# Optimization experiments

Measured on AMD Instinct MI355X. Metric: run time of the kernel, lower is better.

The kernel has to match this reference:

```python
import jax, jax.numpy as jnp
import numpy as np

HIDDEN = 512
B, H, W = 8, 48, 48
SCALE = 1.0 / np.sqrt(HIDDEN).astype(np.float32)


def conv1x1(x, w, b):
    # x: [B, C, H, W], w: [O, C], b: [O]  (1x1 Conv2d == channel matmul)
    return jnp.einsum('bchw,oc->bohw', x, w) + b[None, :, None, None]


def setup_inputs() -> dict:
    key = jax.random.key(0)
    ks = jax.random.split(key, 10)
    s = 1.0 / np.sqrt(HIDDEN)
    return {
        'locx': jax.random.normal(ks[0], (B, HIDDEN, H, W), dtype=jnp.float32),
        'glox': jax.random.normal(ks[1], (B, HIDDEN, H, W), dtype=jnp.float32),
        'Wq': jax.random.normal(ks[2], (HIDDEN, HIDDEN), dtype=jnp.float32) * s,
        'bq': jax.random.normal(ks[3], (HIDDEN,), dtype=jnp.float32) * 0.01,
        'Wk': jax.random.normal(ks[4], (HIDDEN, HIDDEN), dtype=jnp.float32) * s,
        'bk': jax.random.normal(ks[5], (HIDDEN,), dtype=jnp.float32) * 0.01,
        'Wv': jax.random.normal(ks[6], (HIDDEN, HIDDEN), dtype=jnp.float32) * s,
        'bv': jax.random.normal(ks[7], (HIDDEN,), dtype=jnp.float32) * 0.01,
        'Wo': jax.random.normal(ks[8], (HIDDEN, HIDDEN), dtype=jnp.float32) * s,
        'bo': jax.random.normal(ks[9], (HIDDEN,), dtype=jnp.float32) * 0.01,
    }


def reference(locx, glox, Wq, bq, Wk, bk, Wv, bv, Wo, bo):
    b, c, h, w = locx.shape
    # 1x1 conv projections
    q = conv1x1(locx, Wq, bq).reshape(b, c, h * w)   # [B, C, N]
    k = conv1x1(glox, Wk, bk).reshape(b, c, -1)      # [B, C, M]
    v = conv1x1(glox, Wv, bv).reshape(b, c, -1)      # [B, C, M]
    # scores = Q^T K / sqrt(hidden)  -> [B, N, M]
    scores = jnp.einsum('bcn,bcm->bnm', q, k) * SCALE
    probs = jax.nn.softmax(scores, axis=-1)           # dropout rate 0.0 -> identity
    # context = probs @ V^T -> [B, N, C] -> [B, C, H, H]
    ctx = jnp.einsum('bnm,bcm->bcn', probs, v).reshape(b, c, h, h)
    out = conv1x1(ctx, Wo, bo)                        # proj dropout 0.0 -> identity
    return out
```

## Files before the change

### kernel.cpp

```cpp
#include <hip/hip_runtime.h>
#include <hip/hip_bf16.h>

typedef __attribute__((ext_vector_type(4))) float f32x4;
typedef __attribute__((ext_vector_type(8))) short bf16x8;
typedef __attribute__((ext_vector_type(4))) short s16x4;

#define C_DIM 512
#define N_PIX 2304
#define N_BATCH 8
#define ATT_SCALE 0.04419417382415922f
#define NJB 18

typedef __attribute__((address_space(3))) unsigned int lds_u32;
typedef const __attribute__((address_space(1))) unsigned int glob_u32;

__device__ __forceinline__ void gl2lds16(const __hip_bfloat16* g, __hip_bfloat16* l)
{
    __builtin_amdgcn_global_load_lds((glob_u32*)g, (lds_u32*)l, 16, 0, 0);
}

template<int NS>
__global__ __launch_bounds__(256)
void s_vp(const __hip_bfloat16* __restrict__ Qt, const __hip_bfloat16* __restrict__ Kt,
          __hip_bfloat16* __restrict__ Pu, float* __restrict__ rp,
          const __hip_bfloat16* __restrict__ wo, const __hip_bfloat16* __restrict__ Vt,
          __hip_bfloat16* __restrict__ Vp, int bz_off, long sPu)
{
    __shared__ __hip_bfloat16 As[128 * 64];
    __shared__ __hip_bfloat16 Bs[128 * 64];

    const int lin = blockIdx.x;
    const int bz  = lin % NS + bz_off;
    const int t   = lin / NS;
    const bool is_s = (t < 324);

    int ib, jb;
    const __hip_bfloat16 *A, *B;
    __hip_bfloat16* D;
    float scale;
    const long sQ = (long)N_PIX * C_DIM;
    if (is_s) {
        ib = t / 18; jb = t % 18;
        A = Qt + (size_t)bz * sQ;
        B = Kt + (size_t)bz * sQ;
        D = Pu + (size_t)bz * (size_t)sPu;
        scale = ATT_SCALE;
    } else {
        int u = t - 324;
        ib = u / 18; jb = u % 18;
        A = wo;
        B = Vt + (size_t)bz * sQ;
        D = Vp + (size_t)bz * sQ;
        scale = 1.f;
    }
    const int i0 = ib * 128;
    const int j0 = jb * 128;

    const int tid  = threadIdx.x;
    const int lane = tid & 63;
    const int wave = tid >> 6;

    const int lrow = lane >> 3;
    const int lcs  = (lane & 7) ^ lrow;
    const __hip_bfloat16* ga = A + (size_t)(i0 + wave * 32 + lrow) * C_DIM + lcs * 8;
    const __hip_bfloat16* gb = B + (size_t)(j0 + wave * 32 + lrow) * C_DIM + lcs * 8;
    __hip_bfloat16* la = As + wave * 32 * 64;
    __hip_bfloat16* lb = Bs + wave * 32 * 64;

    const int fr = lane & 15;
    const int fq = lane >> 4;
    const int sw = fr & 7;
    const int wi = (wave >> 1) * 64;
    const int wj = (wave & 1) * 64;

    f32x4 acc[4][4];
#pragma unroll
    for (int a = 0; a < 4; ++a)
#pragma unroll
        for (int b = 0; b < 4; ++b)
            acc[a][b] = (f32x4){0.f, 0.f, 0.f, 0.f};

    for (int k0 = 0; k0 < C_DIM; k0 += 64) {
#pragma unroll
        for (int ss = 0; ss < 4; ++ss) {
            gl2lds16(ga + (size_t)ss * 8 * C_DIM + k0, la + ss * 8 * 64);
            gl2lds16(gb + (size_t)ss * 8 * C_DIM + k0, lb + ss * 8 * 64);
        }
        __syncthreads();

#pragma unroll
        for (int kk = 0; kk < 2; ++kk) {
            bf16x8 af[4], bfr[4];
            const int ca = ((kk * 4 + fq) ^ sw) << 3;
#pragma unroll
            for (int tt = 0; tt < 4; ++tt) {
                af[tt]  = *(const bf16x8*)(&As[(wi + tt * 16 + fr) * 64 + ca]);
                bfr[tt] = *(const bf16x8*)(&Bs[(wj + tt * 16 + fr) * 64 + ca]);
            }
#pragma unroll
            for (int a = 0; a < 4; ++a)
#pragma unroll
                for (int b = 0; b < 4; ++b)
                    acc[a][b] = __builtin_amdgcn_mfma_f32_16x16x32_bf16(
                        af[a], bfr[b], acc[a][b], 0, 0, 0);
        }
        __syncthreads();
    }

    const int orow = fq * 4;

    if (is_s) {
        float rpart[4][4];
#pragma unroll
        for (int a = 0; a < 4; ++a)
#pragma unroll
            for (int r = 0; r < 4; ++r)
                rpart[a][r] = 0.f;
#pragma unroll
        for (int a = 0; a < 4; ++a) {
            int ibx = i0 + wi + a * 16 + orow;
#pragma unroll
            for (int b = 0; b < 4; ++b) {
                int j = j0 + wj + b * 16 + fr;
#pragma unroll
                for (int r = 0; r < 4; ++r) {
                    float v = __expf(acc[a][b][r] * scale);
                    rpart[a][r] += v;
                    D[(size_t)(ibx + r) * N_PIX + j] = __float2bfloat16(v);
                }
            }
        }
#pragma unroll
        for (int m = 1; m < 16; m <<= 1)
#pragma unroll
            for (int a = 0; a < 4; ++a)
#pragma unroll
                for (int r = 0; r < 4; ++r)
                    rpart[a][r] += __shfl_xor(rpart[a][r], m);
        float* rsl = (float*)As;
        if (fr == 0) {
#pragma unroll
            for (int a = 0; a < 4; ++a)
#pragma unroll
                for (int r = 0; r < 4; ++r)
                    rsl[wave * 64 + a * 16 + orow + r] = rpart[a][r];
        }
        __syncthreads();
        if (tid < 128) {
            int half = tid >> 6, rr = tid & 63;
            float sm = rsl[(half * 2) * 64 + rr] + rsl[(half * 2 + 1) * 64 + rr];
            rp[((size_t)jb * N_BATCH + bz) * N_PIX + i0 + tid] = sm;
        }
    } else {
#pragma unroll
        for (int a = 0; a < 4; ++a) {
            int ibx = i0 + wi + a * 16 + orow;
#pragma unroll
            for (int b = 0; b < 4; ++b) {
                int j = j0 + wj + b * 16 + fr;
#pragma unroll
                for (int r = 0; r < 4; ++r)
                    D[(size_t)(ibx + r) * N_PIX + j] = __float2bfloat16(acc[a][b][r]);
            }
        }
    }
}

template<int NS>
__global__ __launch_bounds__(256)
void pv_out(const __hip_bfloat16* __restrict__ Vp, const __hip_bfloat16* __restrict__ Pu,
            float* __restrict__ out, const float* __restrict__ bo,
            const float* __restrict__ rp, int bz_off, long sPu)
{
    __shared__ __hip_bfloat16 As[64 * 64];
    __shared__ __hip_bfloat16 Bs[128 * 64];

    const int lin = blockIdx.x;
    const int bz  = lin % NS + bz_off;
    const int t   = lin / NS;
    const int ib  = t % 8;
    const int jb  = t / 8;
    const int i0  = ib * 64;
    const int j0  = jb * 128;

    const long sCN = (long)C_DIM * N_PIX;
    const __hip_bfloat16* A = Vp + (size_t)bz * sCN;
    const __hip_bfloat16* B = Pu + (size_t)bz * (size_t)sPu;
    float* D = out + (size_t)bz * sCN;

    const int tid  = threadIdx.x;
    const int lane = tid & 63;
    const int wave = tid >> 6;

    const int lrow = lane >> 3;
    const int lcs  = (lane & 7) ^ lrow;
    const __hip_bfloat16* ga = A + (size_t)(i0 + wave * 16 + lrow) * N_PIX + lcs * 8;
    const __hip_bfloat16* gb = B + (size_t)(j0 + wave * 32 + lrow) * N_PIX + lcs * 8;
    __hip_bfloat16* la = As + wave * 16 * 64;
    __hip_bfloat16* lb = Bs + wave * 32 * 64;

    const int fr = lane & 15;
    const int fq = lane >> 4;
    const int sw = fr & 7;
    const int wi = (wave >> 1) * 32;
    const int wj = (wave & 1) * 64;

    f32x4 acc[2][4];
#pragma unroll
    for (int a = 0; a < 2; ++a)
#pragma unroll
        for (int b = 0; b < 4; ++b)
            acc[a][b] = (f32x4){0.f, 0.f, 0.f, 0.f};

    for (int k0 = 0; k0 < N_PIX; k0 += 64) {
#pragma unroll
        for (int ss = 0; ss < 2; ++ss)
            gl2lds16(ga + (size_t)ss * 8 * N_PIX + k0, la + ss * 8 * 64);
#pragma unroll
        for (int ss = 0; ss < 4; ++ss)
            gl2lds16(gb + (size_t)ss * 8 * N_PIX + k0, lb + ss * 8 * 64);
        __syncthreads();

#pragma unroll
        for (int kk = 0; kk < 2; ++kk) {
            bf16x8 af[2], bfr[4];
            const int ca = ((kk * 4 + fq) ^ sw) << 3;
#pragma unroll
            for (int tt = 0; tt < 2; ++tt)
                af[tt]  = *(const bf16x8*)(&As[(wi + tt * 16 + fr) * 64 + ca]);
#pragma unroll
            for (int tt = 0; tt < 4; ++tt)
                bfr[tt] = *(const bf16x8*)(&Bs[(wj + tt * 16 + fr) * 64 + ca]);
#pragma unroll
            for (int a = 0; a < 2; ++a)
#pragma unroll
                for (int b = 0; b < 4; ++b)
                    acc[a][b] = __builtin_amdgcn_mfma_f32_16x16x32_bf16(
                        af[a], bfr[b], acc[a][b], 0, 0, 0);
        }
        __syncthreads();
    }

    const int orow = fq * 4;
    float rjv[4];
#pragma unroll
    for (int b = 0; b < 4; ++b) {
        int j = j0 + wj + b * 16 + fr;
        float s = 0.f;
#pragma unroll
        for (int jj = 0; jj < NJB; ++jj)
            s += rp[((size_t)jj * N_BATCH + bz) * N_PIX + j];
        rjv[b] = 1.f / s;
    }

#pragma unroll
    for (int a = 0; a < 2; ++a) {
        int ibx = i0 + wi + a * 16 + orow;
#pragma unroll
        for (int r = 0; r < 4; ++r) {
            float bi = bo[ibx + r];
#pragma unroll
            for (int b = 0; b < 4; ++b) {
                int j = j0 + wj + b * 16 + fr;
                D[(size_t)(ibx + r) * N_PIX + j] = acc[a][b][r] * rjv[b] + bi;
            }
        }
    }
}

__global__ __launch_bounds__(256)
void proj_qkv(const __hip_bfloat16* __restrict__ Xl,
              const __hip_bfloat16* __restrict__ Xg,
              const __hip_bfloat16* __restrict__ wgt,
              const float* __restrict__ bq, const float* __restrict__ bk,
              const float* __restrict__ bv,
              __hip_bfloat16* __restrict__ QKV)
{
    __shared__ __hip_bfloat16 As[128 * 64];
    __shared__ __hip_bfloat16 Bs[128 * 64];

    const int lin = blockIdx.x;
    const int s   = lin % 24;
    const int bz  = s & 7;
    const int mat = s >> 3;
    const int t   = lin / 24;
    const int j0  = (t & 3) * 128;
    const int i0  = (t >> 2) * 128;

    const __hip_bfloat16* Ab = ((mat == 0) ? Xl : Xg) + (size_t)bz * N_PIX * C_DIM;
    const __hip_bfloat16* Bb = wgt + (size_t)mat * C_DIM * C_DIM;
    const float* bias = (mat == 0) ? bq : (mat == 1) ? bk : bv;
    __hip_bfloat16* D = QKV + ((size_t)mat * N_BATCH + bz) * N_PIX * C_DIM;

    const int tid  = threadIdx.x;
    const int lane = tid & 63;
    const int wave = tid >> 6;

    const int lrow = lane >> 3;
    const int lcs  = (lane & 7) ^ lrow;
    const __hip_bfloat16* ga = Ab + (size_t)(i0 + wave * 32 + lrow) * C_DIM + lcs * 8;
    const __hip_bfloat16* gb = Bb + (size_t)(j0 + wave * 32 + lrow) * C_DIM + lcs * 8;
    __hip_bfloat16* la = As + wave * 32 * 64;
    __hip_bfloat16* lb = Bs + wave * 32 * 64;

    const int fr = lane & 15;
    const int fq = lane >> 4;
    const int sw = fr & 7;
    const int wi = (wave >> 1) * 64;
    const int wj = (wave & 1) * 64;

    f32x4 acc[4][4];
#pragma unroll
    for (int a = 0; a < 4; ++a)
#pragma unroll
        for (int b = 0; b < 4; ++b)
            acc[a][b] = (f32x4){0.f, 0.f, 0.f, 0.f};

    for (int k0 = 0; k0 < C_DIM; k0 += 64) {
#pragma unroll
        for (int ss = 0; ss < 4; ++ss) {
            gl2lds16(ga + (size_t)ss * 8 * C_DIM + k0, la + ss * 8 * 64);
            gl2lds16(gb + (size_t)ss * 8 * C_DIM + k0, lb + ss * 8 * 64);
        }
        __syncthreads();

#pragma unroll
        for (int kk = 0; kk < 2; ++kk) {
            bf16x8 af[4], bfr[4];
            const int ca = ((kk * 4 + fq) ^ sw) << 3;
#pragma unroll
            for (int tt = 0; tt < 4; ++tt) {
                af[tt]  = *(const bf16x8*)(&As[(wi + tt * 16 + fr) * 64 + ca]);
                bfr[tt] = *(const bf16x8*)(&Bs[(wj + tt * 16 + fr) * 64 + ca]);
            }
#pragma unroll
            for (int a = 0; a < 4; ++a)
#pragma unroll
                for (int b = 0; b < 4; ++b)
                    acc[a][b] = __builtin_amdgcn_mfma_f32_16x16x32_bf16(
                        af[a], bfr[b], acc[a][b], 0, 0, 0);
        }
        __syncthreads();
    }

    const int orow = fq * 4;
#pragma unroll
    for (int a = 0; a < 4; ++a) {
        int ibx = i0 + wi + a * 16 + orow;
#pragma unroll
        for (int b = 0; b < 4; ++b) {
            int j = j0 + wj + b * 16 + fr;
            float bj = bias[j];
#pragma unroll
            for (int r = 0; r < 4; ++r)
                D[(size_t)(ibx + r) * C_DIM + j] = __float2bfloat16(acc[a][b][r] + bj);
        }
    }
}

__global__ __launch_bounds__(256)
void prep(const float* __restrict__ locx, const float* __restrict__ glox,
          __hip_bfloat16* __restrict__ Xl, __hip_bfloat16* __restrict__ Xg,
          const float* __restrict__ w0, const float* __restrict__ w1,
          const float* __restrict__ w2, const float* __restrict__ w3,
          __hip_bfloat16* __restrict__ wgt)
{
    const int lin = blockIdx.x;
    const int tid = threadIdx.x;

    if (lin < 4608) {
        __shared__ float t[64 * 65];
        const int z  = lin & 15;
        const int t2 = lin >> 4;
        const int c0 = (t2 & 7) * 64;
        const int n0 = (t2 >> 3) * 64;
        const size_t b = z & 7;
        const float* Xb = ((z < 8) ? locx : glox) + b * (size_t)C_DIM * N_PIX;
        __hip_bfloat16* Xt = (z < 8) ? Xl : Xg;

        const int n_l = tid & 63;
        const int c_b = tid >> 6;
#pragma unroll
        for (int s = 0; s < 16; ++s) {
            int c_l = c_b + s * 4;
            t[c_l * 65 + n_l] = Xb[(size_t)(c0 + c_l) * N_PIX + n0 + n_l];
        }
        __syncthreads();

        const int cc = (tid & 7) * 8;
        const int nb = tid >> 3;
#pragma unroll
        for (int it = 0; it < 2; ++it) {
            int n2 = nb + it * 32;
            union { __hip_bfloat16 h[8]; int4 v; } u;
#pragma unroll
            for (int w = 0; w < 8; ++w)
                u.h[w] = __float2bfloat16(t[(cc + w) * 65 + n2]);
            *(int4*)(&Xt[(b * N_PIX + n0 + n2) * C_DIM + c0 + cc]) = u.v;
        }
    } else {
        const int idx = lin - 4608;
        const int w   = idx >> 8;
        const float* srcs[4] = {w0, w1, w2, w3};
        const int i = ((idx & 255) * 256 + tid) * 4;
        float4 f = *(const float4*)(srcs[w] + i);
        union { __hip_bfloat16 h[4]; s16x4 q; } u;
        u.h[0] = __float2bfloat16(f.x);
        u.h[1] = __float2bfloat16(f.y);
        u.h[2] = __float2bfloat16(f.z);
        u.h[3] = __float2bfloat16(f.w);
        *(s16x4*)(wgt + (size_t)w * C_DIM * C_DIM + i) = u.q;
    }
}

extern "C" void kernel_launch(void* const* d_in, const int* in_sizes, int n_in,
                              void* d_out, int out_size, void* d_ws, size_t ws_size,
                              hipStream_t stream)
{
    const float* locx = (const float*)d_in[0];
    const float* glox = (const float*)d_in[1];
    const float* Wq = (const float*)d_in[2];
    const float* bq = (const float*)d_in[3];
    const float* Wk = (const float*)d_in[4];
    const float* bk = (const float*)d_in[5];
    const float* Wv = (const float*)d_in[6];
    const float* bv = (const float*)d_in[7];
    const float* Wo = (const float*)d_in[8];
    const float* bo = (const float*)d_in[9];
    float* out = (float*)d_out;

    const int C = C_DIM, N = N_PIX;
    const size_t WB   = (size_t)C * C * 2;
    const size_t szX  = (size_t)N_BATCH * N * C * 2;
    const size_t szP1 = (size_t)N * N * 2;
    const size_t szRP = (size_t)NJB * N_BATCH * N * 4;

    const size_t fixed = 4 * WB + 6 * szX + szRP;
    bool full = (ws_size >= fixed + 8 * szP1 + 4096);

    char* ws = (char*)d_ws;
    size_t off = 0;
    auto alloc = [&](size_t bytes) {
        char* p = ws + off;
        off += (bytes + 255) & ~(size_t)255;
        return p;
    };
    __hip_bfloat16* wgt = (__hip_bfloat16*)alloc(4 * WB);
    __hip_bfloat16* Xl  = (__hip_bfloat16*)alloc(szX);
    __hip_bfloat16* Xg  = (__hip_bfloat16*)alloc(szX);
    __hip_bfloat16* QKV = (__hip_bfloat16*)alloc(3 * szX);
    __hip_bfloat16* Vp  = (__hip_bfloat16*)alloc(szX);
    float*          rp  = (float*)alloc(szRP);
    __hip_bfloat16* Pu  = (__hip_bfloat16*)alloc(full ? 8 * szP1 : szP1);

    __hip_bfloat16* Qt = QKV;
    __hip_bfloat16* Kt = QKV + (size_t)N_BATCH * N * C;
    __hip_bfloat16* Vt = QKV + 2 * (size_t)N_BATCH * N * C;
    __hip_bfloat16* wo_b = wgt + 3 * (size_t)C * C;

    const dim3 blk(256);

    prep<<<dim3(5632), blk, 0, stream>>>(locx, glox, Xl, Xg, Wq, Wk, Wv, Wo, wgt);
    proj_qkv<<<dim3(24 * 72), blk, 0, stream>>>(Xl, Xg, wgt, bq, bk, bv, QKV);

    if (full) {
        s_vp<8><<<dim3(8 * 396), blk, 0, stream>>>(
            Qt, Kt, Pu, rp, wo_b, Vt, Vp, 0, (long)N * N);
        pv_out<8><<<dim3(8 * 144), blk, 0, stream>>>(
            Vp, Pu, out, bo, rp, 0, (long)N * N);
    } else {
        for (int r = 0; r < N_BATCH; ++r) {
            s_vp<1><<<dim3(396), blk, 0, stream>>>(
                Qt, Kt, Pu, rp, wo_b, Vt, Vp, r, 0);
            pv_out<1><<<dim3(144), blk, 0, stream>>>(
                Vp, Pu, out, bo, rp, r, 0);
        }
    }
}
```

Before: 319.1 us.

## Enlarge score GEMM tiles to 256x256 with double-buffered LDS pipeline

```diff
diff --git a/kernel.cpp b/kernel.cpp
--- a/kernel.cpp
+++ b/kernel.cpp
@@ -9,7 +9,7 @@
 #define N_PIX 2304
 #define N_BATCH 8
 #define ATT_SCALE 0.04419417382415922f
-#define NJB 18
+#define NJB 9
 
 typedef __attribute__((address_space(3))) unsigned int lds_u32;
 typedef const __attribute__((address_space(1))) unsigned int glob_u32;
@@ -19,42 +19,93 @@
     __builtin_amdgcn_global_load_lds((glob_u32*)g, (lds_u32*)l, 16, 0, 0);
 }
 
+
+#define BAR()  __builtin_amdgcn_s_barrier()
+#define LGK0() asm volatile("s_waitcnt lgkmcnt(0)" ::: "memory")
+#define VM4()  asm volatile("s_waitcnt vmcnt(4)" ::: "memory")
+#define VM0()  asm volatile("s_waitcnt vmcnt(0)" ::: "memory")
+#define PRIO(p) __builtin_amdgcn_s_setprio(p)
+
+#define STAGE_A(dd, hh, tk) do { \
+    _Pragma("unroll") \
+    for (int ss = 0; ss < 2; ++ss) { \
+        const int ur0 = wave * 16 + ss * 8; \
+        const int row0 = ((ur0 >> 6) << 7) + (hh) * 64 + (ur0 & 63); \
+        gl2lds16(gA + (size_t)row0 * C_DIM + (tk) * 64, \
+                 (__hip_bfloat16*)&LA[dd][row0 * 64]); \
+    } } while (0)
+
+#define STAGE_B(dd, bb, tk) do { \
+    _Pragma("unroll") \
+    for (int ss = 0; ss < 2; ++ss) { \
+        const int ur0 = wave * 16 + ss * 8; \
+        const int row0 = ((ur0 >> 5) << 6) + (bb) * 32 + (ur0 & 31); \
+        gl2lds16(gB + (size_t)row0 * C_DIM + (tk) * 64, \
+                 (__hip_bfloat16*)&LB[dd][row0 * 64]); \
+    } } while (0)
+
+#define LOAD_A(dd, hh) do { \
+    _Pragma("unroll") \
+    for (int tt = 0; tt < 4; ++tt) { \
+        const int rb = (wr * 128 + (hh) * 64 + tt * 16 + fr) * 64; \
+        _Pragma("unroll") \
+        for (int kk = 0; kk < 2; ++kk) \
+            aF[tt][kk] = *(const bf16x8*)(&LA[dd][rb + (((kk * 4 + fq) ^ sw) << 3)]); \
+    } } while (0)
+
+#define LOAD_B(dd, bb, dst) do { \
+    _Pragma("unroll") \
+    for (int s2 = 0; s2 < 2; ++s2) { \
+        const int rb = (wc * 64 + (bb) * 32 + s2 * 16 + fr) * 64; \
+        _Pragma("unroll") \
+        for (int kk = 0; kk < 2; ++kk) \
+            dst[s2][kk] = *(const bf16x8*)(&LB[dd][rb + (((kk * 4 + fq) ^ sw) << 3)]); \
+    } } while (0)
+
+#define MFMA_Q(HH, BB, bsrc) do { \
+    _Pragma("unroll") \
+    for (int tt = 0; tt < 4; ++tt) \
+    _Pragma("unroll") \
+    for (int s2 = 0; s2 < 2; ++s2) \
+    _Pragma("unroll") \
+    for (int kk = 0; kk < 2; ++kk) \
+        acc[(HH) * 4 + tt][(BB) * 2 + s2] = __builtin_amdgcn_mfma_f32_16x16x32_bf16( \
+            aF[tt][kk], bsrc[s2][kk], acc[(HH) * 4 + tt][(BB) * 2 + s2], 0, 0, 0); \
+    } while (0)
+
 template<int NS>
-__global__ __launch_bounds__(256)
+__global__ __launch_bounds__(512, 2)
 void s_vp(const __hip_bfloat16* __restrict__ Qt, const __hip_bfloat16* __restrict__ Kt,
           __hip_bfloat16* __restrict__ Pu, float* __restrict__ rp,
           const __hip_bfloat16* __restrict__ wo, const __hip_bfloat16* __restrict__ Vt,
           __hip_bfloat16* __restrict__ Vp, int bz_off, long sPu)
 {
-    __shared__ __hip_bfloat16 As[128 * 64];
-    __shared__ __hip_bfloat16 Bs[128 * 64];
+    __shared__ __hip_bfloat16 LA[2][256 * 64];
+    __shared__ __hip_bfloat16 LB[2][256 * 64];
 
     const int lin = blockIdx.x;
     const int bz  = lin % NS + bz_off;
     const int t   = lin / NS;
-    const bool is_s = (t < 324);
+    const bool is_s = (t < 81);
 
     int ib, jb;
     const __hip_bfloat16 *A, *B;
     __hip_bfloat16* D;
-    float scale;
     const long sQ = (long)N_PIX * C_DIM;
     if (is_s) {
-        ib = t / 18; jb = t % 18;
+        ib = t / 9; jb = t % 9;
         A = Qt + (size_t)bz * sQ;
         B = Kt + (size_t)bz * sQ;
         D = Pu + (size_t)bz * (size_t)sPu;
-        scale = ATT_SCALE;
     } else {
-        int u = t - 324;
-        ib = u / 18; jb = u % 18;
+        int u = t - 81;
+        ib = u / 9; jb = u % 9;
         A = wo;
         B = Vt + (size_t)bz * sQ;
         D = Vp + (size_t)bz * sQ;
-        scale = 1.f;
-    }
-    const int i0 = ib * 128;
-    const int j0 = jb * 128;
+    }
+    const int i0 = ib * 256;
+    const int j0 = jb * 256;
 
     const int tid  = threadIdx.x;
     const int lane = tid & 63;
@@ -62,109 +113,157 @@
 
     const int lrow = lane >> 3;
     const int lcs  = (lane & 7) ^ lrow;
-    const __hip_bfloat16* ga = A + (size_t)(i0 + wave * 32 + lrow) * C_DIM + lcs * 8;
-    const __hip_bfloat16* gb = B + (size_t)(j0 + wave * 32 + lrow) * C_DIM + lcs * 8;
-    __hip_bfloat16* la = As + wave * 32 * 64;
-    __hip_bfloat16* lb = Bs + wave * 32 * 64;
+    const __hip_bfloat16* gA = A + (size_t)(i0 + lrow) * C_DIM + lcs * 8;
+    const __hip_bfloat16* gB = B + (size_t)(j0 + lrow) * C_DIM + lcs * 8;
 
     const int fr = lane & 15;
     const int fq = lane >> 4;
     const int sw = fr & 7;
-    const int wi = (wave >> 1) * 64;
-    const int wj = (wave & 1) * 64;
-
-    f32x4 acc[4][4];
-#pragma unroll
-    for (int a = 0; a < 4; ++a)
+    const int wr = wave >> 2;
+    const int wc = wave & 3;
+
+    f32x4 acc[8][4];
+#pragma unroll
+    for (int a = 0; a < 8; ++a)
 #pragma unroll
         for (int b = 0; b < 4; ++b)
             acc[a][b] = (f32x4){0.f, 0.f, 0.f, 0.f};
 
-    for (int k0 = 0; k0 < C_DIM; k0 += 64) {
-#pragma unroll
-        for (int ss = 0; ss < 4; ++ss) {
-            gl2lds16(ga + (size_t)ss * 8 * C_DIM + k0, la + ss * 8 * 64);
-            gl2lds16(gb + (size_t)ss * 8 * C_DIM + k0, lb + ss * 8 * 64);
-        }
-        __syncthreads();
-
-#pragma unroll
-        for (int kk = 0; kk < 2; ++kk) {
-            bf16x8 af[4], bfr[4];
-            const int ca = ((kk * 4 + fq) ^ sw) << 3;
-#pragma unroll
-            for (int tt = 0; tt < 4; ++tt) {
-                af[tt]  = *(const bf16x8*)(&As[(wi + tt * 16 + fr) * 64 + ca]);
-                bfr[tt] = *(const bf16x8*)(&Bs[(wj + tt * 16 + fr) * 64 + ca]);
-            }
-#pragma unroll
-            for (int a = 0; a < 4; ++a)
-#pragma unroll
-                for (int b = 0; b < 4; ++b)
-                    acc[a][b] = __builtin_amdgcn_mfma_f32_16x16x32_bf16(
-                        af[a], bfr[b], acc[a][b], 0, 0, 0);
-        }
-        __syncthreads();
-    }
-
-    const int orow = fq * 4;
+    bf16x8 aF[4][2], bF0[2][2], bF1[2][2];
+
+    STAGE_A(0, 0, 0); STAGE_B(0, 0, 0); STAGE_B(0, 1, 0); STAGE_A(0, 1, 0);
+    STAGE_A(1, 0, 1); STAGE_B(1, 1, 1);
+    VM4();
+    BAR();
+
+    for (int kt = 0; kt < 6; ++kt) {
+        const int d = kt & 1, e = d ^ 1;
+        LOAD_A(d, 0); LOAD_B(d, 0, bF0);
+        STAGE_A(e, 1, kt + 1);
+        BAR(); LGK0();
+        PRIO(1); MFMA_Q(0, 0, bF0); PRIO(0);
+        BAR();
+        LOAD_B(d, 1, bF1);
+        STAGE_B(e, 0, kt + 1);
+        BAR(); LGK0();
+        PRIO(1); MFMA_Q(0, 1, bF1); PRIO(0);
+        BAR();
+        LOAD_A(d, 1);
+        STAGE_A(d, 0, kt + 2);
+        BAR(); LGK0();
+        PRIO(1); MFMA_Q(1, 1, bF1); PRIO(0);
+        BAR();
+        STAGE_B(d, 1, kt + 2);
+        VM4();
+        BAR();
+        PRIO(1); MFMA_Q(1, 0, bF0); PRIO(0);
+        BAR();
+    }
+    {
+        LOAD_A(0, 0); LOAD_B(0, 0, bF0);
+        STAGE_A(1, 1, 7);
+        BAR(); LGK0();
+        PRIO(1); MFMA_Q(0, 0, bF0); PRIO(0);
+        BAR();
+        LOAD_B(0, 1, bF1);
+        STAGE_B(1, 0, 7);
+        BAR(); LGK0();
+        PRIO(1); MFMA_Q(0, 1, bF1); PRIO(0);
+        BAR();
+        LOAD_A(0, 1);
+        BAR(); LGK0();
+        PRIO(1); MFMA_Q(1, 1, bF1); PRIO(0);
+        BAR();
+        VM0();
+        BAR();
+        PRIO(1); MFMA_Q(1, 0, bF0); PRIO(0);
+        BAR();
+    }
+    {
+        LOAD_A(1, 0); LOAD_B(1, 0, bF0);
+        BAR(); LGK0();
+        PRIO(1); MFMA_Q(0, 0, bF0); PRIO(0);
+        BAR();
+        LOAD_B(1, 1, bF1);
+        BAR(); LGK0();
+        PRIO(1); MFMA_Q(0, 1, bF1); PRIO(0);
+        BAR();
+        LOAD_A(1, 1);
+        BAR(); LGK0();
+        PRIO(1); MFMA_Q(1, 1, bF1); PRIO(0);
+        BAR();
+        PRIO(1); MFMA_Q(1, 0, bF0); PRIO(0);
+    }
 
     if (is_s) {
-        float rpart[4][4];
-#pragma unroll
-        for (int a = 0; a < 4; ++a)
+        float rpart[8][4];
+#pragma unroll
+        for (int a = 0; a < 8; ++a)
 #pragma unroll
             for (int r = 0; r < 4; ++r)
                 rpart[a][r] = 0.f;
 #pragma unroll
-        for (int a = 0; a < 4; ++a) {
-            int ibx = i0 + wi + a * 16 + orow;
+        for (int a = 0; a < 8; ++a) {
+            const int grow = i0 + wr * 128 + a * 16 + fq * 4;
 #pragma unroll
             for (int b = 0; b < 4; ++b) {
-                int j = j0 + wj + b * 16 + fr;
+                const int col = j0 + wc * 64 + b * 16 + fr;
 #pragma unroll
                 for (int r = 0; r < 4; ++r) {
-                    float v = __expf(acc[a][b][r] * scale);
+                    float v = __expf(acc[a][b][r] * ATT_SCALE);
                     rpart[a][r] += v;
-                    D[(size_t)(ibx + r) * N_PIX + j] = __float2bfloat16(v);
+                    D[(size_t)(grow + r) * N_PIX + col] = __float2bfloat16(v);
                 }
             }
         }
 #pragma unroll
         for (int m = 1; m < 16; m <<= 1)
 #pragma unroll
-            for (int a = 0; a < 4; ++a)
+            for (int a = 0; a < 8; ++a)
 #pragma unroll
                 for (int r = 0; r < 4; ++r)
                     rpart[a][r] += __shfl_xor(rpart[a][r], m);
-        float* rsl = (float*)As;
+        float* rsl = (float*)&LA[0][0];
+        __syncthreads();
         if (fr == 0) {
 #pragma unroll
-            for (int a = 0; a < 4; ++a)
+            for (int a = 0; a < 8; ++a)
 #pragma unroll
                 for (int r = 0; r < 4; ++r)
-                    rsl[wave * 64 + a * 16 + orow + r] = rpart[a][r];
-        }
-        __syncthreads();
-        if (tid < 128) {
-            int half = tid >> 6, rr = tid & 63;
-            float sm = rsl[(half * 2) * 64 + rr] + rsl[(half * 2 + 1) * 64 + rr];
-            rp[((size_t)jb * N_BATCH + bz) * N_PIX + i0 + tid] = sm;
+                    rsl[wave * 128 + a * 16 + fq * 4 + r] = rpart[a][r];
+        }
+        __syncthreads();
+        if (tid < 256) {
+            const int wr2 = tid >> 7, rl = tid & 127;
+            float s = rsl[(wr2 * 4 + 0) * 128 + rl] + rsl[(wr2 * 4 + 1) * 128 + rl]
+                    + rsl[(wr2 * 4 + 2) * 128 + rl] + rsl[(wr2 * 4 + 3) * 128 + rl];
+            rp[((size_t)jb * N_BATCH + bz) * N_PIX + i0 + tid] = s;
         }
     } else {
 #pragma unroll
-        for (int a = 0; a < 4; ++a) {
-            int ibx = i0 + wi + a * 16 + orow;
+        for (int a = 0; a < 8; ++a) {
+            const int grow = i0 + wr * 128 + a * 16 + fq * 4;
 #pragma unroll
             for (int b = 0; b < 4; ++b) {
-                int j = j0 + wj + b * 16 + fr;
+                const int col = j0 + wc * 64 + b * 16 + fr;
 #pragma unroll
                 for (int r = 0; r < 4; ++r)
-                    D[(size_t)(ibx + r) * N_PIX + j] = __float2bfloat16(acc[a][b][r]);
+                    D[(size_t)(grow + r) * N_PIX + col] = __float2bfloat16(acc[a][b][r]);
             }
         }
     }
 }
+
+#undef STAGE_A
+#undef STAGE_B
+#undef LOAD_A
+#undef LOAD_B
+#undef MFMA_Q
+#undef BAR
+#undef LGK0
+#undef VM4
+#undef VM0
+#undef PRIO
 
 template<int NS>
 __global__ __launch_bounds__(256)
@@ -464,13 +563,13 @@
     proj_qkv<<<dim3(24 * 72), blk, 0, stream>>>(Xl, Xg, wgt, bq, bk, bv, QKV);
 
     if (full) {
-        s_vp<8><<<dim3(8 * 396), blk, 0, stream>>>(
+        s_vp<8><<<dim3(8 * 99), dim3(512), 0, stream>>>(
             Qt, Kt, Pu, rp, wo_b, Vt, Vp, 0, (long)N * N);
         pv_out<8><<<dim3(8 * 144), blk, 0, stream>>>(
             Vp, Pu, out, bo, rp, 0, (long)N * N);
     } else {
         for (int r = 0; r < N_BATCH; ++r) {
-            s_vp<1><<<dim3(396), blk, 0, stream>>>(
+            s_vp<1><<<dim3(99), dim3(512), 0, stream>>>(
                 Qt, Kt, Pu, rp, wo_b, Vt, Vp, r, 0);
             pv_out<1><<<dim3(144), blk, 0, stream>>>(
                 Vp, Pu, out, bo, rp, r, 0);
```

New measurement: 322.8 us. About the same (+1.2%).
